# Optimization experiments

Measured on AMD Instinct MI355X. Metric: run time of the kernel, lower is better.

## Reference

```python
import jax, jax.numpy as jnp
import numpy as np

B, T, C, H = 4, 2048, 1024, 16
D = C // H  # head_dim = 64

def setup_inputs() -> dict:
    key = jax.random.key(0)
    ks = jax.random.split(key, 5)
    scale = 1.0 / np.sqrt(C)
    return {
        "x": jax.random.normal(ks[0], (B, T, C), dtype=jnp.float32),
        "Wq": jax.random.normal(ks[1], (C, C), dtype=jnp.float32) * scale,
        "Wk": jax.random.normal(ks[2], (C, C), dtype=jnp.float32) * scale,
        "Wv": jax.random.normal(ks[3], (C, C), dtype=jnp.float32) * scale,
        "Wo": jax.random.normal(ks[4], (C, C), dtype=jnp.float32) * scale,
        "bo": jnp.zeros((C,), dtype=jnp.float32),
    }

def reference(x, Wq, Wk, Wv, Wo, bo):
    Bx, Tx, Cx = x.shape
    # projections -> [B, H, T, D]
    def split_heads(y):
        return y.reshape(Bx, Tx, H, D).transpose(0, 2, 1, 3)
    Q = split_heads(x @ Wq)
    K = split_heads(x @ Wk)
    V = split_heads(x @ Wv)
    # scaled dot-product with causal mask: [B, H, T, T]
    scores = jnp.einsum('bhqd,bhkd->bhqk', Q, K) / jnp.sqrt(jnp.asarray(D, x.dtype))
    causal = jnp.tril(jnp.ones((Tx, Tx), dtype=bool))
    scores = jnp.where(causal, scores, -jnp.inf)
    weights = jax.nn.softmax(scores, axis=-1)
    attn = jnp.einsum('bhqk,bhkd->bhqd', weights, V)  # [B, H, T, D]
    out = attn.transpose(0, 2, 1, 3).reshape(Bx, Tx, Cx)
    return out @ Wo + bo
```

## Files before the change

### kernel.cpp

```cpp
#include <hip/hip_runtime.h>
#include <hip/hip_bf16.h>
#include <cmath>

typedef __bf16 bf16;
typedef __bf16 bf16x8 __attribute__((ext_vector_type(8)));
typedef __bf16 bf16x4v __attribute__((ext_vector_type(4)));
typedef float f32x4 __attribute__((ext_vector_type(4)));

#define B_ 4
#define T_ 2048
#define C_ 1024
#define H_ 16
#define D_ 64
#define BT_ 8192
#define LOG2E 1.4426950408889634f

__device__ __forceinline__ void async_cp16(const void* g, void* l) {
  __builtin_amdgcn_global_load_lds(
      (__attribute__((address_space(1))) void*)g,
      (__attribute__((address_space(3))) void*)l, 16, 0, 0);
}

__device__ __forceinline__ f32x4 mfma16(bf16x8 a, bf16x8 b, f32x4 c) {
  return __builtin_amdgcn_mfma_f32_16x16x32_bf16(a, b, c, 0, 0, 0);
}

__global__ __launch_bounds__(256) void prep_kernel(
    const float* __restrict__ x, const float* __restrict__ Wq,
    const float* __restrict__ Wk, const float* __restrict__ Wv,
    const float* __restrict__ Wo, bf16* __restrict__ xb,
    bf16* __restrict__ wt) {
  __shared__ float tile[32][33];
  const int id = blockIdx.x;
  const int t = threadIdx.x;
  if (id < 8192) {
    const int i = id * 256 + t;
    float4 v = ((const float4*)x)[i];
    bf16x4v o = {(bf16)v.x, (bf16)v.y, (bf16)v.z, (bf16)v.w};
    ((bf16x4v*)xb)[i] = o;
    return;
  }
  const int id2 = id - 8192;
  const int z = id2 >> 10;
  const float* W = (z == 0) ? Wq : (z == 1) ? Wk : (z == 2) ? Wv : Wo;
  bf16* Wt = wt + (size_t)z * 1048576;
  const int bx = id2 & 31, by = (id2 >> 5) & 31;
  const int xx = t & 31, yy = t >> 5;
  const int n0 = bx * 32, k0 = by * 32;
#pragma unroll
  for (int j = 0; j < 32; j += 8)
    tile[yy + j][xx] = W[(size_t)(k0 + yy + j) * C_ + n0 + xx];
  __syncthreads();
#pragma unroll
  for (int j = 0; j < 32; j += 8)
    Wt[(size_t)(n0 + yy + j) * C_ + k0 + xx] = (bf16)tile[xx][yy + j];
}

template <int F32OUT>
__device__ __forceinline__ void gemm_tile_db(
    const bf16* __restrict__ A, const bf16* __restrict__ Bt,
    void* __restrict__ Cv, const float* __restrict__ bias, int M, int N, int K,
    int m0, int n0, bf16* As, bf16* Bs) {
  const int t = threadIdx.x;
  const int lane = t & 63;
  const int wave = t >> 6;
  const int quad = lane >> 4;
  const int l15 = lane & 15;
  const int l7 = l15 & 7;
  const int wm = (wave >> 1) * 64;
  const int wn = (wave & 1) * 64;

  const int sr8 = lane >> 3;
  const int sc = (lane & 7) ^ sr8;
  const bf16* Ag = A + (size_t)(m0 + wave * 32 + sr8) * K + sc * 8;
  const bf16* Bg = Bt + (size_t)(n0 + wave * 32 + sr8) * K + sc * 8;

  const int niter = K >> 6;
  auto stage = [&](int kt, int buf) {
    bf16* Ad = As + buf * 8192 + wave * 2048 + lane * 8;
    bf16* Bd = Bs + buf * 8192 + wave * 2048 + lane * 8;
#pragma unroll
    for (int i = 0; i < 4; i++) {
      async_cp16(Ag + kt * 64 + (size_t)(i * 8) * K, Ad + i * 512);
      async_cp16(Bg + kt * 64 + (size_t)(i * 8) * K, Bd + i * 512);
    }
  };

  f32x4 acc[4][4] = {};
  stage(0, 0);

  for (int kt = 0; kt < niter; kt++) {
    __syncthreads();
    if (kt + 1 < niter) stage(kt + 1, (kt + 1) & 1);
    const bf16* Ab = As + (kt & 1) * 8192;
    const bf16* Bb = Bs + (kt & 1) * 8192;
#pragma unroll
    for (int ks = 0; ks < 2; ks++) {
      bf16x8 af[4], bfr[4];
#pragma unroll
      for (int i = 0; i < 4; i++)
        af[i] = *(const bf16x8*)&Ab[(wm + i * 16 + l15) * 64 +
                                    (((ks * 4 + quad) ^ l7) * 8)];
#pragma unroll
      for (int j = 0; j < 4; j++)
        bfr[j] = *(const bf16x8*)&Bb[(wn + j * 16 + l15) * 64 +
                                     (((ks * 4 + quad) ^ l7) * 8)];
#pragma unroll
      for (int i = 0; i < 4; i++)
#pragma unroll
        for (int j = 0; j < 4; j++)
          acc[i][j] = mfma16(af[i], bfr[j], acc[i][j]);
    }
  }

#pragma unroll
  for (int i = 0; i < 4; i++) {
    const int gr = m0 + wm + i * 16 + quad * 4;
#pragma unroll
    for (int j = 0; j < 4; j++) {
      const int gc = n0 + wn + j * 16 + l15;
      const float bv = F32OUT ? bias[gc] : 0.0f;
#pragma unroll
      for (int r = 0; r < 4; r++) {
        const float v = acc[i][j][r] + bv;
        if (F32OUT)
          ((float*)Cv)[(size_t)(gr + r) * N + gc] = v;
        else
          ((bf16*)Cv)[(size_t)(gr + r) * N + gc] = (bf16)v;
      }
    }
  }
}

__global__ __launch_bounds__(256, 2) void qkv_gemm_kernel(
    const bf16* __restrict__ xb, const bf16* __restrict__ wqkvT,
    bf16* __restrict__ qkb, bf16* __restrict__ vtb) {
  __shared__ __align__(16) bf16 As[2 * 8192];
  __shared__ __align__(16) bf16 Bs[2 * 8192];
  int id = blockIdx.x;
  if (id < 1024) {
    gemm_tile_db<0>(xb, wqkvT, (void*)qkb, nullptr, 8192, 2048, 1024,
                    (id >> 4) * 128, (id & 15) * 128, As, Bs);
  } else {
    id -= 1024;
    gemm_tile_db<0>(wqkvT + 2 * 1024 * 1024, xb, (void*)vtb, nullptr, 1024,
                    8192, 1024, (id >> 6) * 128, (id & 63) * 128, As, Bs);
  }
}

__global__ __launch_bounds__(256, 2) void out_gemm_kernel(
    const bf16* __restrict__ attn, const bf16* __restrict__ woT,
    float* __restrict__ out, const float* __restrict__ bo) {
  __shared__ __align__(16) bf16 As[2 * 8192];
  __shared__ __align__(16) bf16 Bs[2 * 8192];
  const int id = blockIdx.x;
  gemm_tile_db<1>(attn, woT, (void*)out, bo, 8192, 1024, 1024,
                  (id >> 3) * 128, (id & 7) * 128, As, Bs);
}

__global__ __launch_bounds__(256, 3) void flash_attn_kernel(
    const bf16* __restrict__ qk, const bf16* __restrict__ vt,
    bf16* __restrict__ attn) {
  __shared__ __align__(16) char smem[51200];
  bf16* KsB = (bf16*)smem;
  bf16* VsB = (bf16*)(smem + 16384);
  bf16* Ps = (bf16*)(smem + 32768);

  const int t = threadIdx.x;
  const int lane = t & 63;
  const int wave = t >> 6;
  const int quad = lane >> 4;
  const int l15 = lane & 15;
  const int l7 = l15 & 7;
  const int bx = blockIdx.x;
  const int qt = 15 - (bx >> 6);
  const int bh = bx & 63;
  const int b = bh >> 4;
  const int h = bh & 15;

  const bf16* Qg = qk + (size_t)b * T_ * 2048 + h * 64;
  const bf16* Kg = qk + (size_t)b * T_ * 2048 + 1024 + h * 64;
  const bf16* Vg = vt + (size_t)h * 64 * BT_ + b * T_;

  const float QSCALE = 0.125f * LOG2E;
  bf16x8 qf[2][2];
  const int qrow0 = qt * 128 + wave * 32;
#pragma unroll
  for (int mt = 0; mt < 2; mt++)
#pragma unroll
    for (int ks = 0; ks < 2; ks++) {
      bf16x8 v = *(const bf16x8*)(Qg + (size_t)(qrow0 + mt * 16 + l15) * 2048 +
                                  ks * 32 + quad * 8);
#pragma unroll
      for (int j = 0; j < 8; j++) v[j] = (bf16)((float)v[j] * QSCALE);
      qf[mt][ks] = v;
    }

  f32x4 o_acc[4][2] = {};
  f32x4 l4[2] = {};

  const int sr8 = lane >> 3;
  const int sc = (lane & 7) ^ sr8;

  auto stage = [&](int j64, int buf) {
    const int k0 = j64 * 64;
    bf16* KL = KsB + buf * 4096 + wave * 1024 + lane * 8;
    const bf16* KG = Kg + (size_t)(k0 + wave * 16 + sr8) * 2048 + sc * 8;
    async_cp16(KG, KL);
    async_cp16(KG + (size_t)8 * 2048, KL + 512);
    bf16* VL = VsB + buf * 4096 + wave * 1024 + lane * 8;
    const bf16* VG = Vg + (size_t)(wave * 16 + sr8) * BT_ + k0 + sc * 8;
    async_cp16(VG, VL);
    async_cp16(VG + (size_t)8 * BT_, VL + 512);
  };

  const int S = 2 * qt + 2;
  stage(0, 0);

  for (int s = 0; s < S; s++) {
    __syncthreads();
    if (s + 1 < S) stage(s + 1, (s + 1) & 1);
    const bf16* Kb = KsB + (s & 1) * 4096;
    const bf16* Vb = VsB + (s & 1) * 4096;
    const int k0 = s * 64;
    const bool diag = (s >= 2 * qt);

    bf16x4v p[2][4];
#pragma unroll
    for (int kt = 0; kt < 4; kt++) {
      const bf16x8 kf0 =
          *(const bf16x8*)&Kb[(kt * 16 + l15) * 64 + ((quad ^ l7) * 8)];
      const bf16x8 kf1 =
          *(const bf16x8*)&Kb[(kt * 16 + l15) * 64 + (((4 + quad) ^ l7) * 8)];
#pragma unroll
      for (int mt = 0; mt < 2; mt++) {
        f32x4 sv = mfma16(kf0, qf[mt][0], f32x4{0.f, 0.f, 0.f, 0.f});
        sv = mfma16(kf1, qf[mt][1], sv);
        if (diag) {
          const int qg = qt * 128 + wave * 32 + mt * 16 + l15;
#pragma unroll
          for (int i = 0; i < 4; i++)
            if (k0 + kt * 16 + quad * 4 + i > qg) sv[i] = -INFINITY;
        }
        f32x4 e;
#pragma unroll
        for (int i = 0; i < 4; i++) e[i] = __builtin_amdgcn_exp2f(sv[i]);
        l4[mt] += e;
        p[mt][kt] = bf16x4v{(bf16)e[0], (bf16)e[1], (bf16)e[2], (bf16)e[3]};
      }
    }

#pragma unroll
    for (int mt = 0; mt < 2; mt++) {
      const int row = wave * 32 + mt * 16 + l15;
#pragma unroll
      for (int kt = 0; kt < 4; kt++)
        *(bf16x4v*)&Ps[row * 72 + kt * 16 + quad * 4] = p[mt][kt];
    }

#pragma unroll
    for (int ks2 = 0; ks2 < 2; ks2++) {
      bf16x8 pa[2], vb[4];
#pragma unroll
      for (int mt = 0; mt < 2; mt++)
        pa[mt] = *(const bf16x8*)&Ps[(wave * 32 + mt * 16 + l15) * 72 +
                                     ks2 * 32 + quad * 8];
#pragma unroll
      for (int dt = 0; dt < 4; dt++)
        vb[dt] = *(const bf16x8*)&Vb[(dt * 16 + l15) * 64 +
                                     (((ks2 * 4 + quad) ^ l7) * 8)];
#pragma unroll
      for (int dt = 0; dt < 4; dt++)
#pragma unroll
        for (int mt = 0; mt < 2; mt++)
          o_acc[dt][mt] = mfma16(vb[dt], pa[mt], o_acc[dt][mt]);
    }
  }

  float inv[2];
#pragma unroll
  for (int mt = 0; mt < 2; mt++) {
    float l = l4[mt][0] + l4[mt][1] + l4[mt][2] + l4[mt][3];
    l += __shfl_xor(l, 16, 64);
    l += __shfl_xor(l, 32, 64);
    inv[mt] = 1.0f / l;
  }
#pragma unroll
  for (int dt = 0; dt < 4; dt++)
#pragma unroll
    for (int mt = 0; mt < 2; mt++) {
      const int q = qt * 128 + wave * 32 + mt * 16 + l15;
      bf16x4v o = {(bf16)(o_acc[dt][mt][0] * inv[mt]),
                   (bf16)(o_acc[dt][mt][1] * inv[mt]),
                   (bf16)(o_acc[dt][mt][2] * inv[mt]),
                   (bf16)(o_acc[dt][mt][3] * inv[mt])};
      *(bf16x4v*)(attn + (size_t)(b * T_ + q) * 1024 + h * 64 + dt * 16 +
                  quad * 4) = o;
    }
}

extern "C" void kernel_launch(void* const* d_in, const int* in_sizes, int n_in,
                              void* d_out, int out_size, void* d_ws,
                              size_t ws_size, hipStream_t stream) {
  const float* x = (const float*)d_in[0];
  const float* Wq = (const float*)d_in[1];
  const float* Wk = (const float*)d_in[2];
  const float* Wv = (const float*)d_in[3];
  const float* Wo = (const float*)d_in[4];
  const float* bo = (const float*)d_in[5];
  float* out = (float*)d_out;

  char* ws = (char*)d_ws;
  bf16* xb = (bf16*)(ws);
  bf16* qkb = (bf16*)(ws + 16777216);
  bf16* vtb = (bf16*)(ws + 50331648);
  bf16* attn = (bf16*)(ws + 67108864);
  bf16* wqkvT = (bf16*)(ws + 83886080);

  prep_kernel<<<12288, 256, 0, stream>>>(x, Wq, Wk, Wv, Wo, xb, wqkvT);

  qkv_gemm_kernel<<<1536, 256, 0, stream>>>(xb, wqkvT, qkb, vtb);

  flash_attn_kernel<<<1024, 256, 0, stream>>>(qkb, vtb, attn);

  out_gemm_kernel<<<512, 256, 0, stream>>>(attn, wqkvT + 3 * 1024 * 1024, out,
                                           bo);
}
```

Before: 233.1 us.

## Rewrite QKV GEMM with 256x256 tiles, 8 waves and ping-pong MFMA schedule

Replaces the 128x128 double-buffered QKV projection GEMM with a 256x256-tile, 512-thread kernel. Its K loop interleaves async global-to-LDS staging with barrier-separated MFMA quadrants and raises wave priority around the MFMA clusters. Block IDs are remapped so neighbouring blocks share operand tiles. The larger tile is meant to cut global and LDS traffic per FLOP and keep the matrix cores busy, at the cost of 128 KB of LDS per block, fewer blocks (384), and many barriers.

After: 241.5 us. 1.04x slower.

```diff
diff --git a/kernel.cpp b/kernel.cpp
--- a/kernel.cpp
+++ b/kernel.cpp
@@ -132,19 +132,194 @@
   }
 }
 
-__global__ __launch_bounds__(256, 2) void qkv_gemm_kernel(
+__device__ __forceinline__ void stage256(const bf16* g, bf16* d, int K) {
+#pragma unroll
+  for (int i = 0; i < 4; i++)
+    async_cp16(g + (size_t)(i * 64) * K, d + i * 4096);
+}
+
+__device__ __forceinline__ void read_a4(bf16x8 (&af)[4][2], const bf16* Ab,
+                                        int rowb, int quad, int l7) {
+#pragma unroll
+  for (int f = 0; f < 4; f++)
+#pragma unroll
+    for (int ks = 0; ks < 2; ks++)
+      af[f][ks] = *(const bf16x8*)&Ab[(rowb + f * 16) * 64 +
+                                      (((ks * 4 + quad) ^ l7) * 8)];
+}
+
+__device__ __forceinline__ void read_b2(bf16x8 (&bf)[2][2], const bf16* Bb,
+                                        int rowb, int quad, int l7) {
+#pragma unroll
+  for (int c = 0; c < 2; c++)
+#pragma unroll
+    for (int ks = 0; ks < 2; ks++)
+      bf[c][ks] = *(const bf16x8*)&Bb[(rowb + c * 16) * 64 +
+                                      (((ks * 4 + quad) ^ l7) * 8)];
+}
+
+template <int MH, int NH>
+__device__ __forceinline__ void mfma_quad(f32x4 (&acc)[8][4],
+                                          const bf16x8 (&af)[4][2],
+                                          const bf16x8 (&bf)[2][2]) {
+#pragma unroll
+  for (int f = 0; f < 4; f++)
+#pragma unroll
+    for (int c = 0; c < 2; c++) {
+      f32x4 v = acc[MH * 4 + f][NH * 2 + c];
+      v = mfma16(af[f][0], bf[c][0], v);
+      v = mfma16(af[f][1], bf[c][1], v);
+      acc[MH * 4 + f][NH * 2 + c] = v;
+    }
+}
+
+__device__ __forceinline__ void gemm256(const bf16* __restrict__ A,
+                                        const bf16* __restrict__ Bt,
+                                        bf16* __restrict__ C, int M, int N,
+                                        int K, int m0, int n0, bf16* As,
+                                        bf16* Bs) {
+  const int t = threadIdx.x;
+  const int lane = t & 63;
+  const int wave = t >> 6;
+  const int wm = wave >> 2;
+  const int wn = wave & 3;
+  const int quad = lane >> 4;
+  const int l15 = lane & 15;
+  const int l7 = l15 & 7;
+
+  const int srow = t >> 3;
+  const int schunk = (t & 7) ^ (srow & 7);
+  const bf16* Ag = A + (size_t)(m0 + srow) * K + schunk * 8;
+  const bf16* Bg = Bt + (size_t)(n0 + srow) * K + schunk * 8;
+  bf16* Ad0 = As + t * 8;
+  bf16* Bd0 = Bs + t * 8;
+  bf16* Ad1 = As + 16384 + t * 8;
+  bf16* Bd1 = Bs + 16384 + t * 8;
+
+  const int NI = K >> 7;
+
+  f32x4 acc[8][4] = {};
+  bf16x8 af[4][2], b0[2][2], b1[2][2];
+
+  stage256(Ag, Ad0, K);
+  stage256(Bg, Bd0, K);
+  stage256(Ag + 64, Ad1, K);
+  asm volatile("s_waitcnt vmcnt(4)" ::: "memory");
+  __builtin_amdgcn_s_barrier();
+
+  const int arow = wm * 128 + l15;
+  const int brow = wn * 64 + l15;
+  const bf16* Ab0 = As;
+  const bf16* Bb0 = Bs;
+  const bf16* Ab1 = As + 16384;
+  const bf16* Bb1 = Bs + 16384;
+
+  for (int j = 0; j < NI; j++) {
+    const bool more = (j + 1 < NI);
+    const size_t kb = (size_t)j * 128;
+
+    read_a4(af, Ab0, arow, quad, l7);
+    read_b2(b0, Bb0, brow, quad, l7);
+    stage256(Bg + kb + 64, Bd1, K);
+    __builtin_amdgcn_s_barrier();
+    asm volatile("s_waitcnt lgkmcnt(0)");
+    __builtin_amdgcn_s_setprio(1);
+    mfma_quad<0, 0>(acc, af, b0);
+    __builtin_amdgcn_s_setprio(0);
+    __builtin_amdgcn_s_barrier();
+
+    read_b2(b1, Bb0, brow + 32, quad, l7);
+    __builtin_amdgcn_s_barrier();
+    asm volatile("s_waitcnt lgkmcnt(0)");
+    __builtin_amdgcn_s_setprio(1);
+    mfma_quad<0, 1>(acc, af, b1);
+    __builtin_amdgcn_s_setprio(0);
+    __builtin_amdgcn_s_barrier();
+
+    read_a4(af, Ab0, arow + 64, quad, l7);
+    __builtin_amdgcn_s_barrier();
+    asm volatile("s_waitcnt lgkmcnt(0)");
+    __builtin_amdgcn_s_setprio(1);
+    mfma_quad<1, 1>(acc, af, b1);
+    __builtin_amdgcn_s_setprio(0);
+    __builtin_amdgcn_s_barrier();
+
+    if (more) stage256(Ag + kb + 128, Ad0, K);
+    if (more)
+      asm volatile("s_waitcnt vmcnt(4)" ::: "memory");
+    else
+      asm volatile("s_waitcnt vmcnt(0)" ::: "memory");
+    __builtin_amdgcn_s_barrier();
+    __builtin_amdgcn_s_setprio(1);
+    mfma_quad<1, 0>(acc, af, b0);
+    __builtin_amdgcn_s_setprio(0);
+    __builtin_amdgcn_s_barrier();
+
+    read_a4(af, Ab1, arow, quad, l7);
+    read_b2(b0, Bb1, brow, quad, l7);
+    if (more) stage256(Bg + kb + 128, Bd0, K);
+    __builtin_amdgcn_s_barrier();
+    asm volatile("s_waitcnt lgkmcnt(0)");
+    __builtin_amdgcn_s_setprio(1);
+    mfma_quad<0, 0>(acc, af, b0);
+    __builtin_amdgcn_s_setprio(0);
+    __builtin_amdgcn_s_barrier();
+
+    read_b2(b1, Bb1, brow + 32, quad, l7);
+    __builtin_amdgcn_s_barrier();
+    asm volatile("s_waitcnt lgkmcnt(0)");
+    __builtin_amdgcn_s_setprio(1);
+    mfma_quad<0, 1>(acc, af, b1);
+    __builtin_amdgcn_s_setprio(0);
+    __builtin_amdgcn_s_barrier();
+
+    read_a4(af, Ab1, arow + 64, quad, l7);
+    __builtin_amdgcn_s_barrier();
+    asm volatile("s_waitcnt lgkmcnt(0)");
+    __builtin_amdgcn_s_setprio(1);
+    mfma_quad<1, 1>(acc, af, b1);
+    __builtin_amdgcn_s_setprio(0);
+    __builtin_amdgcn_s_barrier();
+
+    if (more) {
+      stage256(Ag + kb + 192, Ad1, K);
+      asm volatile("s_waitcnt vmcnt(4)" ::: "memory");
+    }
+    __builtin_amdgcn_s_barrier();
+    __builtin_amdgcn_s_setprio(1);
+    mfma_quad<1, 0>(acc, af, b0);
+    __builtin_amdgcn_s_setprio(0);
+    __builtin_amdgcn_s_barrier();
+  }
+
+#pragma unroll
+  for (int f = 0; f < 8; f++) {
+    const int gr = m0 + wm * 128 + f * 16 + quad * 4;
+#pragma unroll
+    for (int c = 0; c < 4; c++) {
+      const int gc = n0 + wn * 64 + c * 16 + l15;
+#pragma unroll
+      for (int r = 0; r < 4; r++)
+        C[(size_t)(gr + r) * N + gc] = (bf16)acc[f][c][r];
+    }
+  }
+}
+
+__global__ __launch_bounds__(512, 2) void qkv_gemm_kernel(
     const bf16* __restrict__ xb, const bf16* __restrict__ wqkvT,
     bf16* __restrict__ qkb, bf16* __restrict__ vtb) {
-  __shared__ __align__(16) bf16 As[2 * 8192];
-  __shared__ __align__(16) bf16 Bs[2 * 8192];
-  int id = blockIdx.x;
-  if (id < 1024) {
-    gemm_tile_db<0>(xb, wqkvT, (void*)qkb, nullptr, 8192, 2048, 1024,
-                    (id >> 4) * 128, (id & 15) * 128, As, Bs);
+  __shared__ __align__(16) bf16 As[2 * 16384];
+  __shared__ __align__(16) bf16 Bs[2 * 16384];
+  const int id = blockIdx.x;
+  if (id < 256) {
+    const int s = (id & 7) * 32 + (id >> 3);
+    gemm256(xb, wqkvT, qkb, 8192, 2048, 1024, (s >> 3) * 256, (s & 7) * 256,
+            As, Bs);
   } else {
-    id -= 1024;
-    gemm_tile_db<0>(wqkvT + 2 * 1024 * 1024, xb, (void*)vtb, nullptr, 1024,
-                    8192, 1024, (id >> 6) * 128, (id & 63) * 128, As, Bs);
+    const int id2 = id - 256;
+    const int s = (id2 & 7) * 16 + (id2 >> 3);
+    gemm256(wqkvT + 2 * 1024 * 1024, xb, vtb, 1024, 8192, 1024,
+            (s >> 5) * 256, (s & 31) * 256, As, Bs);
   }
 }
 
@@ -319,7 +494,7 @@
 
   prep_kernel<<<12288, 256, 0, stream>>>(x, Wq, Wk, Wv, Wo, xb, wqkvT);
 
-  qkv_gemm_kernel<<<1536, 256, 0, stream>>>(xb, wqkvT, qkb, vtb);
+  qkv_gemm_kernel<<<384, 512, 0, stream>>>(xb, wqkvT, qkb, vtb);
 
   flash_attn_kernel<<<1024, 256, 0, stream>>>(qkb, vtb, attn);
 
```
